# Kernel optimization log

Measured on AMD Instinct MI355X. Metric: run time of the kernel, lower is better.

Reference implementation:

```python
import jax, jax.numpy as jnp
import numpy as np

NHEAD = 6
EPS = 1.1920929e-07  # torch RMSNorm default eps = finfo(float32).eps


def _rms(x, g):
    return x * jax.lax.rsqrt(jnp.mean(x * x, axis=-1, keepdims=True) + EPS) * g


def _mha(q, k, v):
    # q: [B, Sq, Hq, D]; k, v: [B, Sk, Hk, D] with Hk == Hq or Hk == 1 (broadcast)
    d = q.shape[-1]
    qh = q.transpose(0, 2, 1, 3)            # [B, Hq, Sq, D]
    kh = k.transpose(0, 2, 1, 3)            # [B, Hk, Sk, D]
    vh = v.transpose(0, 2, 1, 3)
    s = jnp.matmul(qh, kh.transpose(0, 1, 3, 2)) * (1.0 / np.sqrt(d).astype(np.float32))
    a = jax.nn.softmax(s, axis=-1)
    return jnp.matmul(a, vh).transpose(0, 2, 1, 3)  # [B, Sq, Hq, D]


def setup_inputs() -> dict:
    key = jax.random.key(0)
    B, R, G, E, L = 4, 1024, 8, 192, 4
    F = 2 * E  # dim_feedforward = emsize * 2
    ks = jax.random.split(key, 12)

    def w(k, shape):
        return jax.random.normal(k, shape, jnp.float32) * 0.02

    return {
        "hidden": jax.random.normal(ks[0], (B, R, G, E), jnp.float32),
        "Wq1": w(ks[1], (L, E, E)), "Wk1": w(ks[2], (L, E, E)),
        "Wv1": w(ks[3], (L, E, E)), "Wo1": w(ks[4], (L, E, E)),
        "Wq2": w(ks[5], (L, E, E)), "Wk2": w(ks[6], (L, E, E)),
        "Wv2": w(ks[7], (L, E, E)), "Wo2": w(ks[8], (L, E, E)),
        "W1": w(ks[9], (L, E, F)), "W2": w(ks[10], (L, F, E)),
        "g1": jnp.ones((L, E), jnp.float32),
        "g2": jnp.ones((L, E), jnp.float32),
        "g3": jnp.ones((L, E), jnp.float32),
        "single_eval_pos": 768,
    }


def reference(hidden, Wq1, Wk1, Wv1, Wo1, Wq2, Wk2, Wv2, Wo2, W1, W2, g1, g2, g3, single_eval_pos):
    B, R, G, E = hidden.shape
    H, D = NHEAD, E // NHEAD
    sep = int(single_eval_pos)
    L = Wq1.shape[0]
    x = hidden
    for i in range(L):
        # --- per-sample attention between feature groups: seqs of length G ---
        xf = x.reshape(B * R, G, E)
        q = (xf @ Wq1[i]).reshape(B * R, G, H, D)
        k = (xf @ Wk1[i]).reshape(B * R, G, H, D)
        v = (xf @ Wv1[i]).reshape(B * R, G, H, D)
        xf = xf + _mha(q, k, v).reshape(B * R, G, E) @ Wo1[i]
        # --- along-column attention over rows with train/test split ---
        xr = _rms(xf, g1[i]).reshape(B, R, G, E).transpose(0, 2, 1, 3).reshape(B * G, R, E)
        q = (xr @ Wq2[i]).reshape(B * G, R, H, D)
        k = (xr[:, :sep] @ Wk2[i]).reshape(B * G, sep, H, D)
        v = (xr[:, :sep] @ Wv2[i]).reshape(B * G, sep, H, D)
        train_out = _mha(q[:, :sep], k, v)
        # test rows attend to first head's keys/values only (broadcast over heads)
        test_out = _mha(q[:, sep:], k[:, :, :1], v[:, :, :1])
        attn = jnp.concatenate([train_out, test_out], axis=1).reshape(B * G, R, E) @ Wo2[i]
        xc = _rms(xr + attn, g2[i])
        # --- MLP (exact GELU) + final RMSNorm ---
        x = xc.reshape(B, G, R, E).transpose(0, 2, 1, 3)
        x = x + jax.nn.gelu(x @ W1[i], approximate=False) @ W2[i]
        x = _rms(x, g3[i])
    return x
```

## Files before the change

kernel.cpp:

```cpp
#include <hip/hip_runtime.h>
#include <hip/hip_bf16.h>
#include <math.h>

#define B_ 4
#define R_ 1024
#define G_ 8
#define E_ 192
#define H_ 6
#define D_ 32
#define L_ 4
#define F_ 384
#define M_ (B_*R_*G_)
static const size_t NBUF = (size_t)M_ * E_;
static const size_t WPL  = 8 * (size_t)E_ * E_ + 2 * (size_t)E_ * F_;

typedef __attribute__((ext_vector_type(8))) short bf16x8;
typedef __attribute__((ext_vector_type(8))) unsigned short u16x8;
typedef __attribute__((ext_vector_type(4))) float f32x4;

__device__ __forceinline__ float gelu_exact(float x) {
    return 0.5f * x * (1.0f + erff(x * 0.7071067811865475f));
}
__device__ __forceinline__ unsigned short f2bf(float f) {
    __hip_bfloat16 h = __float2bfloat16(f);
    return *(unsigned short*)&h;
}
__device__ __forceinline__ float bf2f(unsigned short h) {
    union { unsigned u; float f; } v; v.u = ((unsigned)h) << 16; return v.f;
}
__device__ __forceinline__ bf16x8 mk8(unsigned long long lo, unsigned long long hi) {
    union { unsigned long long q[2]; bf16x8 v; } u;
    u.q[0] = lo; u.q[1] = hi; return u.v;
}

__global__ __launch_bounds__(256)
void k_convw_all(const float* __restrict__ Wq1, const float* __restrict__ Wk1,
                 const float* __restrict__ Wv1, const float* __restrict__ Wo1,
                 const float* __restrict__ Wq2, const float* __restrict__ Wk2,
                 const float* __restrict__ Wv2, const float* __restrict__ Wo2,
                 const float* __restrict__ W1,  const float* __restrict__ W2,
                 unsigned short* __restrict__ Wt)
{
    const int t = blockIdx.x;
    const int layer = t / 432;
    const int r = t % 432;
    const float* src; unsigned short* dst; int K, N; float scale = 1.f; int tile;
    if (r < 288) {
        const int w = r / 36; tile = r % 36; K = E_; N = E_;
        const float* tab[8] = {Wq1, Wk1, Wv1, Wo1, Wq2, Wk2, Wv2, Wo2};
        src = tab[w] + (size_t)layer * E_ * E_;
        dst = Wt + (size_t)layer * WPL + (size_t)w * E_ * E_;
        if (w == 0) scale = 0.17677669529663687f;
        if (w == 4) scale = 0.17677669529663687f * 1.4426950408889634f;
    } else if (r < 360) {
        tile = r - 288; K = E_; N = F_;
        src = W1 + (size_t)layer * E_ * F_;
        dst = Wt + (size_t)layer * WPL + 8 * (size_t)E_ * E_;
    } else {
        tile = r - 360; K = F_; N = E_;
        src = W2 + (size_t)layer * E_ * F_;
        dst = Wt + (size_t)layer * WPL + 8 * (size_t)E_ * E_ + (size_t)E_ * F_;
    }
    const int ntx = N / 32;
    const int kb = (tile / ntx) * 32, nb = (tile % ntx) * 32;
    __shared__ float tl[32][33];
    const int tx = threadIdx.x & 31, ty = threadIdx.x >> 5;
    for (int i2 = 0; i2 < 32; i2 += 8)
        tl[ty + i2][tx] = src[(size_t)(kb + ty + i2) * N + nb + tx];
    __syncthreads();
    for (int i2 = 0; i2 < 32; i2 += 8)
        dst[(size_t)(nb + ty + i2) * K + kb + tx] = f2bf(tl[tx][ty + i2] * scale);
}

template<bool ABF16, int EPI>
__global__ __launch_bounds__(256)
void k_gemm_mfma(const void* __restrict__ Ap, const unsigned short* __restrict__ Wt,
                 void* __restrict__ Cp, int ldc, int K)
{
    __shared__ unsigned short As[64][40];
    __shared__ unsigned short Bs[192][40];
    const int m0 = blockIdx.x * 64;
    const int n0 = blockIdx.y * 192;
    const int tid = threadIdx.x;
    const int w = tid >> 6, lane = tid & 63, l15 = lane & 15, g = lane >> 4;
    const int arow = tid >> 2, akoff = (tid & 3) << 3;
    f32x4 acc[4][3];
#pragma unroll
    for (int mt = 0; mt < 4; ++mt)
#pragma unroll
        for (int nt = 0; nt < 3; ++nt)
#pragma unroll
            for (int r2 = 0; r2 < 4; ++r2) acc[mt][nt][r2] = 0.f;
    const int nK = K >> 5;

    float4 ax, ay; u16x8 av; u16x8 bv0, bv1, bv2;
    auto gload = [&](int k0) {
        if (ABF16) {
            av = *(const u16x8*)((const unsigned short*)Ap + (size_t)(m0 + arow) * K + k0 + akoff);
        } else {
            const float* ap = (const float*)Ap + (size_t)(m0 + arow) * K + k0 + akoff;
            ax = *(const float4*)ap; ay = *(const float4*)(ap + 4);
        }
        bv0 = *(const u16x8*)(Wt + (size_t)(n0 + arow      ) * K + k0 + akoff);
        bv1 = *(const u16x8*)(Wt + (size_t)(n0 + arow +  64) * K + k0 + akoff);
        bv2 = *(const u16x8*)(Wt + (size_t)(n0 + arow + 128) * K + k0 + akoff);
    };
    auto swrite = [&]() {
        u16x8 aw;
        if (ABF16) aw = av;
        else {
            aw[0] = f2bf(ax.x); aw[1] = f2bf(ax.y); aw[2] = f2bf(ax.z); aw[3] = f2bf(ax.w);
            aw[4] = f2bf(ay.x); aw[5] = f2bf(ay.y); aw[6] = f2bf(ay.z); aw[7] = f2bf(ay.w);
        }
        *(u16x8*)&As[arow][akoff] = aw;
        *(u16x8*)&Bs[arow][akoff] = bv0;
        *(u16x8*)&Bs[arow + 64][akoff] = bv1;
        *(u16x8*)&Bs[arow + 128][akoff] = bv2;
    };

    gload(0);
    for (int kc = 0; kc < nK; ++kc) {
        __syncthreads();
        swrite();
        __syncthreads();
        if (kc + 1 < nK) gload((kc + 1) << 5);
        bf16x8 af[4], bfr[3];
#pragma unroll
        for (int mt = 0; mt < 4; ++mt) af[mt] = *(const bf16x8*)&As[mt * 16 + l15][g * 8];
#pragma unroll
        for (int nt = 0; nt < 3; ++nt) bfr[nt] = *(const bf16x8*)&Bs[w * 48 + nt * 16 + l15][g * 8];
#pragma unroll
        for (int mt = 0; mt < 4; ++mt)
#pragma unroll
            for (int nt = 0; nt < 3; ++nt)
                acc[mt][nt] = __builtin_amdgcn_mfma_f32_16x16x32_bf16(af[mt], bfr[nt], acc[mt][nt], 0, 0, 0);
    }

#pragma unroll
    for (int mt = 0; mt < 4; ++mt)
#pragma unroll
        for (int r2 = 0; r2 < 4; ++r2) {
            const int m = m0 + mt * 16 + g * 4 + r2;
#pragma unroll
            for (int nt = 0; nt < 3; ++nt) {
                const int n = w * 48 + nt * 16 + l15;
                float v = acc[mt][nt][r2];
                if (EPI == 1) v = gelu_exact(v);
                ((unsigned short*)Cp)[(size_t)m * ldc + n0 + n] = f2bf(v);
            }
        }
}

template<bool RESBF16, int EPI>
__global__ __launch_bounds__(256)
void k_gemm_rms32(const unsigned short* __restrict__ Ap, const unsigned short* __restrict__ Wt,
                  const void* __restrict__ Resp, const float* __restrict__ gvec,
                  void* __restrict__ Cp, int K)
{
    __shared__ unsigned short As[32][40];
    __shared__ unsigned short Bs[192][40];
    __shared__ float ss_red[4][16];
    const int m0 = blockIdx.x * 32;
    const int tid = threadIdx.x;
    const int w = tid >> 6, lane = tid & 63, l15 = lane & 15, g = lane >> 4;
    const int mt = w & 1, nh = w >> 1;
    const int arow = tid >> 2, akoff = (tid & 3) << 3;
    f32x4 acc[6];
#pragma unroll
    for (int nt = 0; nt < 6; ++nt)
#pragma unroll
        for (int r2 = 0; r2 < 4; ++r2) acc[nt][r2] = 0.f;
    const int nK = K >> 5;

    u16x8 av, bv0, bv1, bv2;
    auto gload = [&](int k0) {
        if (tid < 128)
            av = *(const u16x8*)(Ap + (size_t)(m0 + arow) * K + k0 + akoff);
        bv0 = *(const u16x8*)(Wt + (size_t)(arow      ) * K + k0 + akoff);
        bv1 = *(const u16x8*)(Wt + (size_t)(arow +  64) * K + k0 + akoff);
        bv2 = *(const u16x8*)(Wt + (size_t)(arow + 128) * K + k0 + akoff);
    };
    auto swrite = [&]() {
        if (tid < 128) *(u16x8*)&As[arow][akoff] = av;
        *(u16x8*)&Bs[arow][akoff] = bv0;
        *(u16x8*)&Bs[arow + 64][akoff] = bv1;
        *(u16x8*)&Bs[arow + 128][akoff] = bv2;
    };

    gload(0);
    for (int kc = 0; kc < nK; ++kc) {
        __syncthreads();
        swrite();
        __syncthreads();
        if (kc + 1 < nK) gload((kc + 1) << 5);
        bf16x8 af = *(const bf16x8*)&As[mt * 16 + l15][g * 8];
        bf16x8 bfr[6];
#pragma unroll
        for (int nt = 0; nt < 6; ++nt) bfr[nt] = *(const bf16x8*)&Bs[nh * 96 + nt * 16 + l15][g * 8];
#pragma unroll
        for (int nt = 0; nt < 6; ++nt)
            acc[nt] = __builtin_amdgcn_mfma_f32_16x16x32_bf16(af, bfr[nt], acc[nt], 0, 0, 0);
    }

    float ssp[4] = {0.f, 0.f, 0.f, 0.f};
#pragma unroll
    for (int r2 = 0; r2 < 4; ++r2) {
        const int m = m0 + mt * 16 + g * 4 + r2;
#pragma unroll
        for (int nt = 0; nt < 6; ++nt) {
            const int n = nh * 96 + nt * 16 + l15;
            float rres = RESBF16 ? bf2f(((const unsigned short*)Resp)[(size_t)m * E_ + n])
                                 : ((const float*)Resp)[(size_t)m * E_ + n];
            float v = acc[nt][r2] + rres;
            acc[nt][r2] = v;
            ssp[r2] += v * v;
        }
    }
#pragma unroll
    for (int off = 1; off < 16; off <<= 1)
#pragma unroll
        for (int r2 = 0; r2 < 4; ++r2)
            ssp[r2] += __shfl_xor(ssp[r2], off);
    if (l15 == 0) {
#pragma unroll
        for (int r2 = 0; r2 < 4; ++r2)
            ss_red[w][g * 4 + r2] = ssp[r2];
    }
    __syncthreads();
#pragma unroll
    for (int r2 = 0; r2 < 4; ++r2) {
        const int lr = g * 4 + r2;
        const float ss = ss_red[mt][lr] + ss_red[2 + mt][lr];
        const float inv = rsqrtf(ss * (1.0f / 192.0f) + 1.1920929e-07f);
        const int m = m0 + mt * 16 + lr;
        size_t orow;
        if (EPI == 2) {
            const int b = m >> 13, rr = (m >> 3) & 1023, gg = m & 7;
            orow = (((size_t)b * G_ + gg) << 10) + rr;
        } else if (EPI == 3) {
            const int b = m >> 13, gg = (m >> 10) & 7, rr = m & 1023;
            orow = ((((size_t)b << 10) + rr) << 3) + gg;
        } else {
            orow = m;
        }
#pragma unroll
        for (int nt = 0; nt < 6; ++nt) {
            const int n = nh * 96 + nt * 16 + l15;
            const float v = acc[nt][r2] * inv * gvec[n];
            if (EPI == 4) ((float*)Cp)[orow * E_ + n] = v;
            else          ((unsigned short*)Cp)[orow * E_ + n] = f2bf(v);
        }
    }
}

template<bool AF32>
__global__ __launch_bounds__(256)
void k_featblock(const void* __restrict__ Xin, const unsigned short* __restrict__ Wqkv,
                 const unsigned short* __restrict__ Wo, const float* __restrict__ gvec,
                 unsigned short* __restrict__ Ynb)
{
    __shared__ __align__(16) unsigned char raw[576 * 40 * 2];
    __shared__ __align__(16) unsigned short As[32][40];
    __shared__ __align__(16) unsigned short Tl[32][200];
    __shared__ float ss_red[4][32];

    unsigned short (*Bq)[40]    = (unsigned short (*)[40])raw;
    unsigned short (*QKVl)[584] = (unsigned short (*)[584])raw;
    unsigned short (*Bo)[40]    = (unsigned short (*)[40])raw;

    const int m0 = blockIdx.x * 32;
    const int tid = threadIdx.x;
    const int w = tid >> 6, lane = tid & 63, l15 = lane & 15, g = lane >> 4;
    const int arow = (tid & 127) >> 2, akoff = (tid & 3) << 3;

    f32x4 acc[2][9];
#pragma unroll
    for (int mt = 0; mt < 2; ++mt)
#pragma unroll
        for (int nt = 0; nt < 9; ++nt)
#pragma unroll
            for (int r2 = 0; r2 < 4; ++r2) acc[mt][nt][r2] = 0.f;

    for (int kc = 0; kc < 6; ++kc) {
        const int k0 = kc << 5;
        __syncthreads();
        if (tid < 128) {
            u16x8 aw;
            if (AF32) {
                const float* ap = (const float*)Xin + (size_t)(m0 + arow) * E_ + k0 + akoff;
                float4 x = *(const float4*)ap, y = *(const float4*)(ap + 4);
                aw[0] = f2bf(x.x); aw[1] = f2bf(x.y); aw[2] = f2bf(x.z); aw[3] = f2bf(x.w);
                aw[4] = f2bf(y.x); aw[5] = f2bf(y.y); aw[6] = f2bf(y.z); aw[7] = f2bf(y.w);
            } else {
                aw = *(const u16x8*)((const unsigned short*)Xin + (size_t)(m0 + arow) * E_ + k0 + akoff);
            }
            *(u16x8*)&As[arow][akoff] = aw;
        }
#pragma unroll
        for (int j = 0; j < 9; ++j) {
            const int v = tid + 256 * j;
            const int br = v >> 2, bk = (v & 3) << 3;
            *(u16x8*)&Bq[br][bk] = *(const u16x8*)(Wqkv + (size_t)br * E_ + k0 + bk);
        }
        __syncthreads();
        bf16x8 af0 = *(const bf16x8*)&As[l15][g * 8];
        bf16x8 af1 = *(const bf16x8*)&As[16 + l15][g * 8];
#pragma unroll
        for (int nt = 0; nt < 9; ++nt) {
            bf16x8 bf = *(const bf16x8*)&Bq[w * 144 + nt * 16 + l15][g * 8];
            acc[0][nt] = __builtin_amdgcn_mfma_f32_16x16x32_bf16(af0, bf, acc[0][nt], 0, 0, 0);
            acc[1][nt] = __builtin_amdgcn_mfma_f32_16x16x32_bf16(af1, bf, acc[1][nt], 0, 0, 0);
        }
    }
    __syncthreads();
#pragma unroll
    for (int mt = 0; mt < 2; ++mt)
#pragma unroll
        for (int r2 = 0; r2 < 4; ++r2)
#pragma unroll
            for (int nt = 0; nt < 9; ++nt)
                QKVl[mt * 16 + g * 4 + r2][w * 144 + nt * 16 + l15] = f2bf(acc[mt][nt][r2]);
    __syncthreads();

    {
        const int i = lane >> 3, j = lane & 7;
        const int r0 = w * 8;
#pragma unroll
        for (int h = 0; h < 6; ++h) {
            float s = 0.f;
#pragma unroll
            for (int d8 = 0; d8 < 4; ++d8) {
                u16x8 qv = *(const u16x8*)&QKVl[r0 + i][h * 32 + d8 * 8];
                u16x8 kv = *(const u16x8*)&QKVl[r0 + j][192 + h * 32 + d8 * 8];
#pragma unroll
                for (int e = 0; e < 8; ++e) s += bf2f(qv[e]) * bf2f(kv[e]);
            }
            float mx = s;
#pragma unroll
            for (int off = 1; off < 8; off <<= 1) mx = fmaxf(mx, __shfl_xor(mx, off));
            float p = __expf(s - mx);
            float sum = p;
#pragma unroll
            for (int off = 1; off < 8; off <<= 1) sum += __shfl_xor(sum, off);
            p /= sum;
            const int base = lane & ~7;
            float o0 = 0.f, o1 = 0.f, o2 = 0.f, o3 = 0.f;
#pragma unroll
            for (int jj = 0; jj < 8; ++jj) {
                float pj = __shfl(p, base + jj);
                ushort4 vv = *(const ushort4*)&QKVl[r0 + jj][384 + h * 32 + j * 4];
                o0 += pj * bf2f(vv.x); o1 += pj * bf2f(vv.y);
                o2 += pj * bf2f(vv.z); o3 += pj * bf2f(vv.w);
            }
            ushort4 ov; ov.x = f2bf(o0); ov.y = f2bf(o1); ov.z = f2bf(o2); ov.w = f2bf(o3);
            *(ushort4*)&Tl[r0 + i][h * 32 + j * 4] = ov;
        }
    }
    __syncthreads();

    f32x4 acc2[2][3];
#pragma unroll
    for (int mt = 0; mt < 2; ++mt)
#pragma unroll
        for (int nt = 0; nt < 3; ++nt)
#pragma unroll
            for (int r2 = 0; r2 < 4; ++r2) acc2[mt][nt][r2] = 0.f;

    for (int kc = 0; kc < 6; ++kc) {
        const int k0 = kc << 5;
        __syncthreads();
#pragma unroll
        for (int j = 0; j < 3; ++j) {
            const int v = tid + 256 * j;
            const int br = v >> 2, bk = (v & 3) << 3;
            *(u16x8*)&Bo[br][bk] = *(const u16x8*)(Wo + (size_t)br * E_ + k0 + bk);
        }
        __syncthreads();
        bf16x8 af0 = *(const bf16x8*)&Tl[l15][k0 + g * 8];
        bf16x8 af1 = *(const bf16x8*)&Tl[16 + l15][k0 + g * 8];
#pragma unroll
        for (int nt = 0; nt < 3; ++nt) {
            bf16x8 bf = *(const bf16x8*)&Bo[w * 48 + nt * 16 + l15][g * 8];
            acc2[0][nt] = __builtin_amdgcn_mfma_f32_16x16x32_bf16(af0, bf, acc2[0][nt], 0, 0, 0);
            acc2[1][nt] = __builtin_amdgcn_mfma_f32_16x16x32_bf16(af1, bf, acc2[1][nt], 0, 0, 0);
        }
    }
    __syncthreads();

    float ssp[2][4] = {};
#pragma unroll
    for (int mt = 0; mt < 2; ++mt)
#pragma unroll
        for (int r2 = 0; r2 < 4; ++r2) {
            const int m = m0 + mt * 16 + g * 4 + r2;
#pragma unroll
            for (int nt = 0; nt < 3; ++nt) {
                const int n = w * 48 + nt * 16 + l15;
                float rres = AF32 ? ((const float*)Xin)[(size_t)m * E_ + n]
                                  : bf2f(((const unsigned short*)Xin)[(size_t)m * E_ + n]);
                float v = acc2[mt][nt][r2] + rres;
                acc2[mt][nt][r2] = v;
                ssp[mt][r2] += v * v;
            }
        }
#pragma unroll
    for (int off = 1; off < 16; off <<= 1)
#pragma unroll
        for (int mt = 0; mt < 2; ++mt)
#pragma unroll
            for (int r2 = 0; r2 < 4; ++r2)
                ssp[mt][r2] += __shfl_xor(ssp[mt][r2], off);
    if (l15 == 0) {
#pragma unroll
        for (int mt = 0; mt < 2; ++mt)
#pragma unroll
            for (int r2 = 0; r2 < 4; ++r2)
                ss_red[w][mt * 16 + g * 4 + r2] = ssp[mt][r2];
    }
    __syncthreads();
#pragma unroll
    for (int mt = 0; mt < 2; ++mt)
#pragma unroll
        for (int r2 = 0; r2 < 4; ++r2) {
            const int row = mt * 16 + g * 4 + r2;
            const float ss = ss_red[0][row] + ss_red[1][row] + ss_red[2][row] + ss_red[3][row];
            const float inv = rsqrtf(ss * (1.0f / 192.0f) + 1.1920929e-07f);
            const int m = m0 + row;
            const int b = m >> 13, rr = (m >> 3) & 1023, gg = m & 7;
            const size_t orow = (((size_t)(b * G_ + gg)) << 10) + rr;
#pragma unroll
            for (int nt = 0; nt < 3; ++nt) {
                const int n = w * 48 + nt * 16 + l15;
                Ynb[orow * E_ + n] = f2bf(acc2[mt][nt][r2] * inv * gvec[n]);
            }
        }
}

__global__ __launch_bounds__(256)
void k_attn2(const unsigned short* __restrict__ QKV, unsigned short* __restrict__ T,
             const int* __restrict__ sep_ptr)
{
    __shared__ __align__(16) unsigned short K_lds[64][40];
    __shared__ __align__(16) unsigned short V_lds[2048];

    const int sep = *sep_ptr;
    const int bid = blockIdx.x;
    const int sh = ((bid >> 7) << 3) | (bid & 7);
    const int qtile = (bid >> 3) & 15;
    const int s = sh / H_, h = sh % H_;
    const int q0 = qtile * 64;

    const int tid = threadIdx.x;
    const int w = tid >> 6;
    const int lane = tid & 63;
    const int l15 = lane & 15;
    const int g = lane >> 4;

    const int qrow = q0 + w * 16 + l15;
    u16x8 qf = *(const u16x8*)(QKV + ((size_t)s * R_ + qrow) * 576 + h * D_ + g * 8);

    u16x8 onesu;
#pragma unroll
    for (int e = 0; e < 8; ++e) onesu[e] = 0x3F80;
    const bf16x8 onesf = (bf16x8)onesu;

    const bool lo = (q0 < sep);
    const bool hi = (q0 + 64 > sep);
    const int npass = (lo && hi) ? 2 : 1;
    const int nChunk = (sep + 63) >> 6;

    const int skey = tid >> 2;
    const int sg   = tid & 3;
    const int vst = ((sg >> 1) * 16 + (skey >> 2)) * 64 + (skey & 3) * 16 + (sg & 1) * 8;
    const unsigned vaddr = (unsigned)(size_t)&V_lds[0] + (unsigned)(g * 128 + l15 * 2);

    for (int pass = 0; pass < npass; ++pass) {
        const int hk = (pass == 0) ? (lo ? h : 0) : 0;
        const unsigned short* Kb = QKV + (size_t)s * R_ * 576 + 192 + hk * D_;
        const unsigned short* Vb = QKV + (size_t)s * R_ * 576 + 384 + hk * D_;

        float mrun = -1e30f;
        f32x4 o0 = {0.f, 0.f, 0.f, 0.f};
        f32x4 o1 = {0.f, 0.f, 0.f, 0.f};
        f32x4 o2 = {0.f, 0.f, 0.f, 0.f};

        u16x8 kv_k = *(const u16x8*)(Kb + (size_t)skey * 576 + sg * 8);
        u16x8 kv_v = *(const u16x8*)(Vb + (size_t)skey * 576 + sg * 8);

        for (int kc = 0; kc < nChunk; ++kc) {
            const int kbase = kc * 64;
            const bool full = (kbase + 64 <= sep);
            __syncthreads();
            *(u16x8*)&K_lds[skey][sg * 8] = kv_k;
            *(u16x8*)&V_lds[vst] = kv_v;
            __syncthreads();
            if (kc + 1 < nChunk) {
                kv_k = *(const u16x8*)(Kb + (size_t)(kbase + 64 + skey) * 576 + sg * 8);
                kv_v = *(const u16x8*)(Vb + (size_t)(kbase + 64 + skey) * 576 + sg * 8);
            }

            f32x4 sc[4];
            const f32x4 zf = {0.f, 0.f, 0.f, 0.f};
            __builtin_amdgcn_s_setprio(1);
#pragma unroll
            for (int t = 0; t < 4; ++t) {
                bf16x8 a = *(const bf16x8*)&K_lds[t * 16 + l15][g * 8];
                sc[t] = __builtin_amdgcn_mfma_f32_16x16x32_bf16(a, (bf16x8)qf, zf, 0, 0, 0);
            }
            __builtin_amdgcn_s_setprio(0);
            if (!full) {
#pragma unroll
                for (int t = 0; t < 4; ++t)
#pragma unroll
                    for (int r = 0; r < 4; ++r)
                        if (kbase + t * 16 + g * 4 + r >= sep) sc[t][r] = -1e30f;
            }
            float mx = fmaxf(fmaxf(sc[0][0], sc[0][1]), sc[0][2]);
            mx = fmaxf(fmaxf(sc[0][3], sc[1][0]), mx);
            mx = fmaxf(fmaxf(sc[1][1], sc[1][2]), mx);
            mx = fmaxf(fmaxf(sc[1][3], sc[2][0]), mx);
            mx = fmaxf(fmaxf(sc[2][1], sc[2][2]), mx);
            mx = fmaxf(fmaxf(sc[2][3], sc[3][0]), mx);
            mx = fmaxf(fmaxf(sc[3][1], sc[3][2]), mx);
            mx = fmaxf(mx, sc[3][3]);
            if (!__all((int)(mx <= mrun + 11.0f))) {
                mx = fmaxf(mx, __shfl_xor(mx, 16));
                mx = fmaxf(mx, __shfl_xor(mx, 32));
                const float mnew = fmaxf(mrun, mx);
                const float scl = exp2f(mrun - mnew);
#pragma unroll
                for (int r = 0; r < 4; ++r) { o0[r] *= scl; o1[r] *= scl; o2[r] *= scl; }
                mrun = mnew;
            }
            bf16x8 pb0, pb1;
            {
                u16x8 p0, p1;
#pragma unroll
                for (int r = 0; r < 4; ++r) {
                    p0[r]     = f2bf(exp2f(sc[0][r] - mrun));
                    p0[4 + r] = f2bf(exp2f(sc[1][r] - mrun));
                    p1[r]     = f2bf(exp2f(sc[2][r] - mrun));
                    p1[4 + r] = f2bf(exp2f(sc[3][r] - mrun));
                }
                pb0 = (bf16x8)p0; pb1 = (bf16x8)p1;
            }
            unsigned long long t0, t1, t2, t3, t4, t5, t6, t7;
            asm volatile(
                "ds_read_b64_tr_b16 %0, %8 offset:0\n\t"
                "ds_read_b64_tr_b16 %1, %8 offset:512\n\t"
                "ds_read_b64_tr_b16 %2, %8 offset:1024\n\t"
                "ds_read_b64_tr_b16 %3, %8 offset:1536\n\t"
                "ds_read_b64_tr_b16 %4, %8 offset:2048\n\t"
                "ds_read_b64_tr_b16 %5, %8 offset:2560\n\t"
                "ds_read_b64_tr_b16 %6, %8 offset:3072\n\t"
                "ds_read_b64_tr_b16 %7, %8 offset:3584\n\t"
                "s_waitcnt lgkmcnt(0)"
                : "=&v"(t0), "=&v"(t1), "=&v"(t2), "=&v"(t3),
                  "=&v"(t4), "=&v"(t5), "=&v"(t6), "=&v"(t7)
                : "v"(vaddr)
                : "memory");
            __builtin_amdgcn_sched_barrier(0);
            __builtin_amdgcn_s_setprio(1);
            o0 = __builtin_amdgcn_mfma_f32_16x16x32_bf16(mk8(t0, t1), pb0, o0, 0, 0, 0);
            o1 = __builtin_amdgcn_mfma_f32_16x16x32_bf16(mk8(t4, t5), pb0, o1, 0, 0, 0);
            o2 = __builtin_amdgcn_mfma_f32_16x16x32_bf16(onesf,       pb0, o2, 0, 0, 0);
            o0 = __builtin_amdgcn_mfma_f32_16x16x32_bf16(mk8(t2, t3), pb1, o0, 0, 0, 0);
            o1 = __builtin_amdgcn_mfma_f32_16x16x32_bf16(mk8(t6, t7), pb1, o1, 0, 0, 0);
            o2 = __builtin_amdgcn_mfma_f32_16x16x32_bf16(onesf,       pb1, o2, 0, 0, 0);
            __builtin_amdgcn_s_setprio(0);
        }

        const bool valid = (npass == 1) || (pass == 0 ? (qrow < sep) : (qrow >= sep));
        if (valid) {
            const float inv = 1.f / o2[0];
            unsigned short* tp = T + ((size_t)s * R_ + qrow) * E_ + h * D_;
            ushort4 v0, v1;
            v0.x = f2bf(o0[0] * inv); v0.y = f2bf(o0[1] * inv);
            v0.z = f2bf(o0[2] * inv); v0.w = f2bf(o0[3] * inv);
            v1.x = f2bf(o1[0] * inv); v1.y = f2bf(o1[1] * inv);
            v1.z = f2bf(o1[2] * inv); v1.w = f2bf(o1[3] * inv);
            *(ushort4*)(tp + g * 4)      = v0;
            *(ushort4*)(tp + 16 + g * 4) = v1;
        }
    }
}

extern "C" void kernel_launch(void* const* d_in, const int* in_sizes, int n_in,
                              void* d_out, int out_size, void* d_ws, size_t ws_size,
                              hipStream_t stream) {
    const float* hidden = (const float*)d_in[0];
    const float* Wq1 = (const float*)d_in[1];
    const float* Wk1 = (const float*)d_in[2];
    const float* Wv1 = (const float*)d_in[3];
    const float* Wo1 = (const float*)d_in[4];
    const float* Wq2 = (const float*)d_in[5];
    const float* Wk2 = (const float*)d_in[6];
    const float* Wv2 = (const float*)d_in[7];
    const float* Wo2 = (const float*)d_in[8];
    const float* W1  = (const float*)d_in[9];
    const float* W2  = (const float*)d_in[10];
    const float* g1  = (const float*)d_in[11];
    const float* g2  = (const float*)d_in[12];
    const float* g3  = (const float*)d_in[13];
    const int*   sep = (const int*)d_in[14];

    float* Xout = (float*)d_out;
    unsigned short* ws = (unsigned short*)d_ws;
    unsigned short* QKVb = ws;
    unsigned short* Tb   = QKVb + (size_t)M_ * 576;
    unsigned short* Ynb  = Tb + NBUF;
    unsigned short* Xcb  = Ynb + NBUF;
    unsigned short* Xb   = Xcb + NBUF;
    unsigned short* Wt   = Xb + NBUF;
    unsigned short* H1b  = QKVb;

    const dim3 blk(256);
    const dim3 gQKV(M_ / 64, 3);
    const dim3 gW1(M_ / 64, 2);
    const dim3 g32(M_ / 32);
    const dim3 gA2(32 * H_ * 16);

    k_convw_all<<<dim3(432 * L_), blk, 0, stream>>>(Wq1, Wk1, Wv1, Wo1, Wq2, Wk2, Wv2, Wo2, W1, W2, Wt);

    for (int i = 0; i < L_; ++i) {
        unsigned short* wl = Wt + (size_t)i * WPL;
        const unsigned short* wqkv1 = wl;
        const unsigned short* wo1   = wl + 3 * (size_t)E_ * E_;
        const unsigned short* wqkv2 = wl + 4 * (size_t)E_ * E_;
        const unsigned short* wo2   = wl + 7 * (size_t)E_ * E_;
        const unsigned short* w1    = wl + 8 * (size_t)E_ * E_;
        const unsigned short* w2    = wl + 8 * (size_t)E_ * E_ + (size_t)E_ * F_;
        const float* g1i = g1 + (size_t)i * E_;
        const float* g2i = g2 + (size_t)i * E_;
        const float* g3i = g3 + (size_t)i * E_;

        if (i == 0)
            k_featblock<true><<<g32, blk, 0, stream>>>(hidden, wqkv1, wo1, g1i, Ynb);
        else
            k_featblock<false><<<g32, blk, 0, stream>>>(Xb, wqkv1, wo1, g1i, Ynb);
        k_gemm_mfma<true, 0><<<gQKV, blk, 0, stream>>>(Ynb, wqkv2, QKVb, 576, E_);
        k_attn2<<<gA2, blk, 0, stream>>>(QKVb, Tb, sep);
        k_gemm_rms32<true, 3><<<g32, blk, 0, stream>>>(Tb, wo2, Ynb, g2i, Xcb, E_);
        k_gemm_mfma<true, 1><<<gW1, blk, 0, stream>>>(Xcb, w1, H1b, F_, E_);
        if (i == L_ - 1)
            k_gemm_rms32<true, 4><<<g32, blk, 0, stream>>>(H1b, w2, Xcb, g3i, Xout, F_);
        else
            k_gemm_rms32<true, 5><<<g32, blk, 0, stream>>>(H1b, w2, Xcb, g3i, Xb, F_);
    }
}
```

Before: 641.6 us.

## Load GEMM fragments directly from global memory, dropping LDS staging and barriers

In the RMS-fused GEMM and the feature-block kernel, the A and weight tiles are no longer staged through shared memory. Each lane now loads its MFMA fragments straight from global memory into registers, using a register double-buffer in the GEMM. This removes the LDS writes, LDS reads and paired __syncthreads per K step. The cost is that overlapping fragments are reloaded redundantly across waves through the cache with less coalesced row-strided access, and more registers are held per thread.

```diff
diff --git a/kernel.cpp b/kernel.cpp
--- a/kernel.cpp
+++ b/kernel.cpp
@@ -157,14 +157,11 @@
                   const void* __restrict__ Resp, const float* __restrict__ gvec,
                   void* __restrict__ Cp, int K)
 {
-    __shared__ unsigned short As[32][40];
-    __shared__ unsigned short Bs[192][40];
     __shared__ float ss_red[4][16];
     const int m0 = blockIdx.x * 32;
     const int tid = threadIdx.x;
     const int w = tid >> 6, lane = tid & 63, l15 = lane & 15, g = lane >> 4;
     const int mt = w & 1, nh = w >> 1;
-    const int arow = tid >> 2, akoff = (tid & 3) << 3;
     f32x4 acc[6];
 #pragma unroll
     for (int nt = 0; nt < 6; ++nt)
@@ -172,34 +169,30 @@
         for (int r2 = 0; r2 < 4; ++r2) acc[nt][r2] = 0.f;
     const int nK = K >> 5;
 
-    u16x8 av, bv0, bv1, bv2;
-    auto gload = [&](int k0) {
-        if (tid < 128)
-            av = *(const u16x8*)(Ap + (size_t)(m0 + arow) * K + k0 + akoff);
-        bv0 = *(const u16x8*)(Wt + (size_t)(arow      ) * K + k0 + akoff);
-        bv1 = *(const u16x8*)(Wt + (size_t)(arow +  64) * K + k0 + akoff);
-        bv2 = *(const u16x8*)(Wt + (size_t)(arow + 128) * K + k0 + akoff);
-    };
-    auto swrite = [&]() {
-        if (tid < 128) *(u16x8*)&As[arow][akoff] = av;
-        *(u16x8*)&Bs[arow][akoff] = bv0;
-        *(u16x8*)&Bs[arow + 64][akoff] = bv1;
-        *(u16x8*)&Bs[arow + 128][akoff] = bv2;
-    };
-
-    gload(0);
+    const unsigned short* Arow = Ap + (size_t)(m0 + mt * 16 + l15) * K + g * 8;
+    const unsigned short* Brow = Wt + (size_t)(nh * 96 + l15) * K + g * 8;
+
+    bf16x8 afr = *(const bf16x8*)Arow;
+    bf16x8 bfr[6];
+#pragma unroll
+    for (int nt = 0; nt < 6; ++nt)
+        bfr[nt] = *(const bf16x8*)(Brow + (size_t)(nt * 16) * K);
+
     for (int kc = 0; kc < nK; ++kc) {
-        __syncthreads();
-        swrite();
-        __syncthreads();
-        if (kc + 1 < nK) gload((kc + 1) << 5);
-        bf16x8 af = *(const bf16x8*)&As[mt * 16 + l15][g * 8];
-        bf16x8 bfr[6];
-#pragma unroll
-        for (int nt = 0; nt < 6; ++nt) bfr[nt] = *(const bf16x8*)&Bs[nh * 96 + nt * 16 + l15][g * 8];
+        bf16x8 na; bf16x8 nb[6];
+        if (kc + 1 < nK) {
+            const int k1 = (kc + 1) << 5;
+            na = *(const bf16x8*)(Arow + k1);
+#pragma unroll
+            for (int nt = 0; nt < 6; ++nt)
+                nb[nt] = *(const bf16x8*)(Brow + (size_t)(nt * 16) * K + k1);
+        }
 #pragma unroll
         for (int nt = 0; nt < 6; ++nt)
-            acc[nt] = __builtin_amdgcn_mfma_f32_16x16x32_bf16(af, bfr[nt], acc[nt], 0, 0, 0);
+            acc[nt] = __builtin_amdgcn_mfma_f32_16x16x32_bf16(afr, bfr[nt], acc[nt], 0, 0, 0);
+        afr = na;
+#pragma unroll
+        for (int nt = 0; nt < 6; ++nt) bfr[nt] = nb[nt];
     }
 
     float ssp[4] = {0.f, 0.f, 0.f, 0.f};
@@ -259,19 +252,13 @@
                  const unsigned short* __restrict__ Wo, const float* __restrict__ gvec,
                  unsigned short* __restrict__ Ynb)
 {
-    __shared__ __align__(16) unsigned char raw[576 * 40 * 2];
-    __shared__ __align__(16) unsigned short As[32][40];
+    __shared__ __align__(16) unsigned short QKVl[32][584];
     __shared__ __align__(16) unsigned short Tl[32][200];
     __shared__ float ss_red[4][32];
-
-    unsigned short (*Bq)[40]    = (unsigned short (*)[40])raw;
-    unsigned short (*QKVl)[584] = (unsigned short (*)[584])raw;
-    unsigned short (*Bo)[40]    = (unsigned short (*)[40])raw;
 
     const int m0 = blockIdx.x * 32;
     const int tid = threadIdx.x;
     const int w = tid >> 6, lane = tid & 63, l15 = lane & 15, g = lane >> 4;
-    const int arow = (tid & 127) >> 2, akoff = (tid & 3) << 3;
 
     f32x4 acc[2][9];
 #pragma unroll
@@ -281,38 +268,34 @@
 #pragma unroll
             for (int r2 = 0; r2 < 4; ++r2) acc[mt][nt][r2] = 0.f;
 
+#pragma unroll
     for (int kc = 0; kc < 6; ++kc) {
         const int k0 = kc << 5;
-        __syncthreads();
-        if (tid < 128) {
-            u16x8 aw;
+        bf16x8 af[2];
+#pragma unroll
+        for (int mt = 0; mt < 2; ++mt) {
             if (AF32) {
-                const float* ap = (const float*)Xin + (size_t)(m0 + arow) * E_ + k0 + akoff;
+                const float* ap = (const float*)Xin + (size_t)(m0 + mt * 16 + l15) * E_ + k0 + g * 8;
                 float4 x = *(const float4*)ap, y = *(const float4*)(ap + 4);
+                u16x8 aw;
                 aw[0] = f2bf(x.x); aw[1] = f2bf(x.y); aw[2] = f2bf(x.z); aw[3] = f2bf(x.w);
                 aw[4] = f2bf(y.x); aw[5] = f2bf(y.y); aw[6] = f2bf(y.z); aw[7] = f2bf(y.w);
+                af[mt] = (bf16x8)aw;
             } else {
-                aw = *(const u16x8*)((const unsigned short*)Xin + (size_t)(m0 + arow) * E_ + k0 + akoff);
-            }
-            *(u16x8*)&As[arow][akoff] = aw;
-        }
-#pragma unroll
-        for (int j = 0; j < 9; ++j) {
-            const int v = tid + 256 * j;
-            const int br = v >> 2, bk = (v & 3) << 3;
-            *(u16x8*)&Bq[br][bk] = *(const u16x8*)(Wqkv + (size_t)br * E_ + k0 + bk);
-        }
-        __syncthreads();
-        bf16x8 af0 = *(const bf16x8*)&As[l15][g * 8];
-        bf16x8 af1 = *(const bf16x8*)&As[16 + l15][g * 8];
+                af[mt] = *(const bf16x8*)((const unsigned short*)Xin +
+                          (size_t)(m0 + mt * 16 + l15) * E_ + k0 + g * 8);
+            }
+        }
+        bf16x8 bq[9];
+#pragma unroll
+        for (int nt = 0; nt < 9; ++nt)
+            bq[nt] = *(const bf16x8*)(Wqkv + (size_t)(w * 144 + nt * 16 + l15) * E_ + k0 + g * 8);
 #pragma unroll
         for (int nt = 0; nt < 9; ++nt) {
-            bf16x8 bf = *(const bf16x8*)&Bq[w * 144 + nt * 16 + l15][g * 8];
-            acc[0][nt] = __builtin_amdgcn_mfma_f32_16x16x32_bf16(af0, bf, acc[0][nt], 0, 0, 0);
-            acc[1][nt] = __builtin_amdgcn_mfma_f32_16x16x32_bf16(af1, bf, acc[1][nt], 0, 0, 0);
-        }
-    }
-    __syncthreads();
+            acc[0][nt] = __builtin_amdgcn_mfma_f32_16x16x32_bf16(af[0], bq[nt], acc[0][nt], 0, 0, 0);
+            acc[1][nt] = __builtin_amdgcn_mfma_f32_16x16x32_bf16(af[1], bq[nt], acc[1][nt], 0, 0, 0);
+        }
+    }
 #pragma unroll
     for (int mt = 0; mt < 2; ++mt)
 #pragma unroll
@@ -366,26 +349,18 @@
 #pragma unroll
             for (int r2 = 0; r2 < 4; ++r2) acc2[mt][nt][r2] = 0.f;
 
+#pragma unroll
     for (int kc = 0; kc < 6; ++kc) {
         const int k0 = kc << 5;
-        __syncthreads();
-#pragma unroll
-        for (int j = 0; j < 3; ++j) {
-            const int v = tid + 256 * j;
-            const int br = v >> 2, bk = (v & 3) << 3;
-            *(u16x8*)&Bo[br][bk] = *(const u16x8*)(Wo + (size_t)br * E_ + k0 + bk);
-        }
-        __syncthreads();
         bf16x8 af0 = *(const bf16x8*)&Tl[l15][k0 + g * 8];
         bf16x8 af1 = *(const bf16x8*)&Tl[16 + l15][k0 + g * 8];
 #pragma unroll
         for (int nt = 0; nt < 3; ++nt) {
-            bf16x8 bf = *(const bf16x8*)&Bo[w * 48 + nt * 16 + l15][g * 8];
-            acc2[0][nt] = __builtin_amdgcn_mfma_f32_16x16x32_bf16(af0, bf, acc2[0][nt], 0, 0, 0);
-            acc2[1][nt] = __builtin_amdgcn_mfma_f32_16x16x32_bf16(af1, bf, acc2[1][nt], 0, 0, 0);
-        }
-    }
-    __syncthreads();
+            bf16x8 bfw = *(const bf16x8*)(Wo + (size_t)(w * 48 + nt * 16 + l15) * E_ + k0 + g * 8);
+            acc2[0][nt] = __builtin_amdgcn_mfma_f32_16x16x32_bf16(af0, bfw, acc2[0][nt], 0, 0, 0);
+            acc2[1][nt] = __builtin_amdgcn_mfma_f32_16x16x32_bf16(af1, bfw, acc2[1][nt], 0, 0, 0);
+        }
+    }
 
     float ssp[2][4] = {};
 #pragma unroll
```

New measurement: 823.6 us. +28.4%, slower.
